# Kernel optimization log

Hardware: AMD Instinct MI355X
Metric: run time of the kernel (lower is better)

## Reference

```python
import jax, jax.numpy as jnp
import numpy as np

D_MODEL = 2048
N_HEADS = 16
N_KV_HEADS = 2
HEAD_DIM = D_MODEL // N_HEADS  # 128
N_REP = N_HEADS // N_KV_HEADS  # 8
SCALE = HEAD_DIM ** -0.5


def setup_inputs() -> dict:
    key = jax.random.key(0)
    ks = jax.random.split(key, 5)
    B, N = 2, 2048
    x = jax.random.normal(ks[0], (B, N, D_MODEL), dtype=jnp.float32)
    # weights stored as [in, out] (math identical to torch Linear x @ W.T)
    s = D_MODEL ** -0.5
    Wq = jax.random.normal(ks[1], (D_MODEL, D_MODEL), dtype=jnp.float32) * s
    Wk = jax.random.normal(ks[2], (D_MODEL, N_KV_HEADS * HEAD_DIM), dtype=jnp.float32) * s
    Wv = jax.random.normal(ks[3], (D_MODEL, N_KV_HEADS * HEAD_DIM), dtype=jnp.float32) * s
    Wo = jax.random.normal(ks[4], (D_MODEL, D_MODEL), dtype=jnp.float32) * s
    return {"x": x, "Wq": Wq, "Wk": Wk, "Wv": Wv, "Wo": Wo}


def reference(x, Wq, Wk, Wv, Wo):
    B, N, C = x.shape
    q = (x @ Wq).reshape(B, N, N_HEADS, HEAD_DIM).transpose(0, 2, 1, 3)      # [B,H,N,hd]
    k = (x @ Wk).reshape(B, N, N_KV_HEADS, HEAD_DIM).transpose(0, 2, 1, 3)   # [B,Hkv,N,hd]
    v = (x @ Wv).reshape(B, N, N_KV_HEADS, HEAD_DIM).transpose(0, 2, 1, 3)
    if N_REP > 1:
        k = jnp.repeat(k, N_REP, axis=1)  # [B,H,N,hd]
        v = jnp.repeat(v, N_REP, axis=1)
    attn = jnp.einsum('bhnd,bhmd->bhnm', q, k) * SCALE
    attn = jax.nn.softmax(attn, axis=-1)
    out = jnp.einsum('bhnm,bhmd->bhnd', attn, v)
    out = out.transpose(0, 2, 1, 3).reshape(B, N, C)
    return out @ Wo
```

## Files before the change

kernel.cpp:

```cpp
#include <hip/hip_runtime.h>

typedef unsigned short u16;
typedef __attribute__((ext_vector_type(4))) float floatx4;
typedef __attribute__((ext_vector_type(8))) __bf16 bf16x8;
typedef __attribute__((ext_vector_type(8))) u16 u16x8;

#define D_MODEL 2048
#define SEQ     2048
#define NH      16
#define NKV     2
#define HD      128
#define QKVN    2560
#define SCALE   0.08838834764831845f
#define QSCALE  (0.08838834764831845f * 1.4426950408889634f)
#define M_STATIC 20.0f

__device__ __forceinline__ u16 f2bf(float f) {
    unsigned int x = __float_as_uint(f);
    return (u16)((x + 0x7fffu + ((x >> 16) & 1u)) >> 16);
}
__device__ __forceinline__ u16 cvt_scale(float f, float s) { return f2bf(f * s); }
__device__ __forceinline__ u16 cvt_scale(u16 f, float)     { return f; }

__device__ __forceinline__ void gload16(const u16* g, u16* l) {
    __builtin_amdgcn_global_load_lds((const __attribute__((address_space(1))) void*)g,
                                     (__attribute__((address_space(3))) void*)l, 16, 0, 0);
}

__global__ void f2b_k(const float* __restrict__ src, u16* __restrict__ dst, long n)
{
    long i = ((long)blockIdx.x * blockDim.x + threadIdx.x) * 8;
    if (i >= n) return;
    float4 a = *(const float4*)(src + i);
    float4 b = *(const float4*)(src + i + 4);
    u16x8 o;
    o[0] = f2bf(a.x); o[1] = f2bf(a.y); o[2] = f2bf(a.z); o[3] = f2bf(a.w);
    o[4] = f2bf(b.x); o[5] = f2bf(b.y); o[6] = f2bf(b.z); o[7] = f2bf(b.w);
    *(u16x8*)(dst + i) = o;
}

template <typename T>
__global__ void tr_k(const T* __restrict__ src, u16* __restrict__ dst,
                     int ld_s, int ld_d, long sbs, long dbs, float scale)
{
    __shared__ T tile[32][33];
    src += (long)blockIdx.z * sbs;
    dst += (long)blockIdx.z * dbs;
    int c0 = blockIdx.x * 32, r0 = blockIdx.y * 32;
    int tx = threadIdx.x, ty = threadIdx.y;
#pragma unroll
    for (int i = 0; i < 32; i += 8)
        tile[ty + i][tx] = src[(long)(r0 + ty + i) * ld_s + c0 + tx];
    __syncthreads();
#pragma unroll
    for (int i = 0; i < 32; i += 8)
        dst[(long)(c0 + ty + i) * ld_d + r0 + tx] = cvt_scale(tile[tx][ty + i], scale);
}

template <bool F32OUT>
__global__ __launch_bounds__(256, 2) void gemm_bt_k(
    const u16* __restrict__ A, const u16* __restrict__ Bt, void* __restrict__ Cv,
    int K, int lda, int ldb, int ldc)
{
    __shared__ __align__(16) u16 As[128 * 64];
    __shared__ __align__(16) u16 Bs[128 * 64];
    const int tid  = threadIdx.x;
    const int wave = tid >> 6, lane = tid & 63;
    const int quad = lane >> 4, l16 = lane & 15;
    const long bm = (long)blockIdx.x * 128;
    const long bn = (long)blockIdx.y * 128;
    const int wr = (wave >> 1) * 64;
    const int wc = (wave & 1) * 64;

    floatx4 acc[4][4] = {};

    for (long k0 = 0; k0 < K; k0 += 64) {
#pragma unroll
        for (int t = 0; t < 4; ++t) {
            int c = tid + t * 256;
            int row = c >> 3, sl = c & 7;
            int kc = sl ^ (row & 7);
            gload16(A + (bm + row) * lda + k0 + kc * 8,
                    As + ((tid & ~63) + t * 256) * 8);
        }
#pragma unroll
        for (int t = 0; t < 4; ++t) {
            int c = tid + t * 256;
            int row = c >> 3, sl = c & 7;
            int kc = sl ^ (row & 7);
            gload16(Bt + (bn + row) * ldb + k0 + kc * 8,
                    Bs + ((tid & ~63) + t * 256) * 8);
        }
        __syncthreads();

#pragma unroll
        for (int ks = 0; ks < 2; ++ks) {
            bf16x8 af[4], bfr[4];
#pragma unroll
            for (int mt = 0; mt < 4; ++mt) {
                int r  = wr + mt * 16 + l16;
                int ch = (ks * 4 + quad) ^ (r & 7);
                af[mt] = *(const bf16x8*)(As + r * 64 + ch * 8);
            }
#pragma unroll
            for (int nt = 0; nt < 4; ++nt) {
                int r  = wc + nt * 16 + l16;
                int ch = (ks * 4 + quad) ^ (r & 7);
                bfr[nt] = *(const bf16x8*)(Bs + r * 64 + ch * 8);
            }
#pragma unroll
            for (int mt = 0; mt < 4; ++mt)
#pragma unroll
                for (int nt = 0; nt < 4; ++nt)
                    acc[mt][nt] = __builtin_amdgcn_mfma_f32_16x16x32_bf16(
                        af[mt], bfr[nt], acc[mt][nt], 0, 0, 0);
        }
        __syncthreads();
    }

#pragma unroll
    for (int mt = 0; mt < 4; ++mt)
#pragma unroll
        for (int nt = 0; nt < 4; ++nt)
#pragma unroll
            for (int r = 0; r < 4; ++r) {
                long row = bm + wr + mt * 16 + quad * 4 + r;
                long col = bn + wc + nt * 16 + l16;
                if (F32OUT) ((float*)Cv)[row * ldc + col] = acc[mt][nt][r];
                else        ((u16*)Cv)[row * ldc + col]   = f2bf(acc[mt][nt][r]);
            }
}

#define KTILE (64 * 128)
#define VTILE (128 * 64)
#define NT    (SEQ / 64)

__global__ __launch_bounds__(512, 2) void attn_k(
    const u16* __restrict__ QKV, const u16* __restrict__ Vt, u16* __restrict__ Out)
{
    __shared__ __align__(16) u16 smem[2 * KTILE + 2 * VTILE + 256 * 64];

    const int tid  = threadIdx.x;
    const int wave = tid >> 6, lane = tid & 63;
    const int quad = lane >> 4, l16 = lane & 15;
    const int qs = wave & 3;
    const int hf = wave >> 2;
    const int qt = blockIdx.x, h = blockIdx.y, b = blockIdx.z;
    const int kvh = h >> 3;

    const long qrow0 = (long)b * SEQ + (long)qt * 256;
    const u16* Qbase = QKV + qrow0 * QKVN + h * HD;
    const u16* Kbase = QKV + (long)b * SEQ * QKVN + D_MODEL + kvh * HD;
    const u16* Vbase = Vt + ((long)b * NKV + kvh) * (long)HD * SEQ;
    u16* const P = smem + 2 * KTILE + 2 * VTILE;

#pragma unroll
    for (int t = 0; t < 8; ++t) {
        int c = tid + t * 512;
        int row = c >> 4, sl = c & 15;
        int dc = sl ^ (row & 15);
        gload16(Qbase + (long)row * QKVN + dc * 8, smem + ((tid & ~63) + t * 512) * 8);
    }
    __syncthreads();

    bf16x8 qa[4][4];
#pragma unroll
    for (int mt = 0; mt < 4; ++mt)
#pragma unroll
        for (int ks = 0; ks < 4; ++ks) {
            int r  = qs * 64 + mt * 16 + l16;
            int ch = (ks * 4 + quad) ^ (r & 15);
            qa[mt][ks] = *(const bf16x8*)(smem + r * 128 + ch * 8);
        }
    __syncthreads();

    floatx4 o[4][4] = {};
    float l_run[4] = { 0.f, 0.f, 0.f, 0.f };

    {
        u16* Kn = smem;
        u16* Vn = smem + 2 * KTILE;
#pragma unroll
        for (int t = 0; t < 2; ++t) {
            int c = tid + t * 512;
            int row = c >> 4, sl = c & 15;
            int dc = sl ^ (row & 15);
            gload16(Kbase + (long)row * QKVN + dc * 8, Kn + ((tid & ~63) + t * 512) * 8);
        }
#pragma unroll
        for (int t = 0; t < 2; ++t) {
            int c = tid + t * 512;
            int row = c >> 3, sl = c & 7;
            int kc = sl ^ (row & 7);
            gload16(Vbase + (long)row * SEQ + kc * 8, Vn + ((tid & ~63) + t * 512) * 8);
        }
    }
    __syncthreads();

    for (int t = 0; t < NT; ++t) {
        const int cur = t & 1;
        const u16* Kc = smem + cur * KTILE;
        const u16* Vc = smem + 2 * KTILE + cur * VTILE;

        if (t + 1 < NT) {
            u16* Kn = smem + (cur ^ 1) * KTILE;
            u16* Vn = smem + 2 * KTILE + (cur ^ 1) * VTILE;
            const long k0n = (long)(t + 1) * 64;
#pragma unroll
            for (int tt = 0; tt < 2; ++tt) {
                int c = tid + tt * 512;
                int row = c >> 4, sl = c & 15;
                int dc = sl ^ (row & 15);
                gload16(Kbase + (k0n + row) * QKVN + dc * 8,
                        Kn + ((tid & ~63) + tt * 512) * 8);
            }
#pragma unroll
            for (int tt = 0; tt < 2; ++tt) {
                int c = tid + tt * 512;
                int row = c >> 3, sl = c & 7;
                int kc = sl ^ (row & 7);
                gload16(Vbase + (long)row * SEQ + k0n + kc * 8,
                        Vn + ((tid & ~63) + tt * 512) * 8);
            }
        }

        floatx4 s[4][2] = {};
        __builtin_amdgcn_s_setprio(1);
#pragma unroll
        for (int ks = 0; ks < 4; ++ks) {
            bf16x8 kb[2];
#pragma unroll
            for (int nt = 0; nt < 2; ++nt) {
                int r  = hf * 32 + nt * 16 + l16;
                int ch = (ks * 4 + quad) ^ (r & 15);
                kb[nt] = *(const bf16x8*)(Kc + r * 128 + ch * 8);
            }
#pragma unroll
            for (int mt = 0; mt < 4; ++mt)
#pragma unroll
                for (int nt = 0; nt < 2; ++nt)
                    s[mt][nt] = __builtin_amdgcn_mfma_f32_16x16x32_bf16(
                        kb[nt], qa[mt][ks], s[mt][nt], 0, 0, 0);
        }
        __builtin_amdgcn_s_setprio(0);

#pragma unroll
        for (int mt = 0; mt < 4; ++mt) {
#pragma unroll
            for (int nt = 0; nt < 2; ++nt)
#pragma unroll
                for (int r = 0; r < 4; ++r)
                    s[mt][nt][r] = __builtin_amdgcn_exp2f(s[mt][nt][r] - M_STATIC);
            float ta = (s[mt][0][0] + s[mt][0][1]) + (s[mt][0][2] + s[mt][0][3]);
            float tb = (s[mt][1][0] + s[mt][1][1]) + (s[mt][1][2] + s[mt][1][3]);
            float sum = ta + tb;
            sum += __shfl_xor(sum, 16);
            sum += __shfl_xor(sum, 32);
            l_run[mt] += sum;

            int row = qs * 64 + mt * 16 + l16;
            int m = row & 7;
            u16* base = P + row * 64 + (quad & 1) * 4;
#pragma unroll
            for (int nt = 0; nt < 2; ++nt) {
                unsigned int lo, hi;
                asm("v_cvt_pk_bf16_f32 %0, %1, %2"
                    : "=v"(lo) : "v"(s[mt][nt][0]), "v"(s[mt][nt][1]));
                asm("v_cvt_pk_bf16_f32 %0, %1, %2"
                    : "=v"(hi) : "v"(s[mt][nt][2]), "v"(s[mt][nt][3]));
                int chunk = (hf * 4 + nt * 2 + (quad >> 1)) ^ m;
                uint2 val; val.x = lo; val.y = hi;
                *(uint2*)(base + chunk * 8) = val;
            }
        }

        asm volatile("s_waitcnt lgkmcnt(0)" ::: "memory");
        __builtin_amdgcn_sched_barrier(0);
        __builtin_amdgcn_s_barrier();

        __builtin_amdgcn_s_setprio(1);
#pragma unroll
        for (int ks = 0; ks < 2; ++ks) {
            bf16x8 pa[4];
#pragma unroll
            for (int mt = 0; mt < 4; ++mt) {
                int row = qs * 64 + mt * 16 + l16;
                int chk = (ks * 4 + quad) ^ (row & 7);
                pa[mt] = *(const bf16x8*)(P + row * 64 + chk * 8);
            }
#pragma unroll
            for (int dt = 0; dt < 4; ++dt) {
                int r  = hf * 64 + dt * 16 + l16;
                int ch = (ks * 4 + quad) ^ (r & 7);
                bf16x8 vb = *(const bf16x8*)(Vc + r * 64 + ch * 8);
#pragma unroll
                for (int mt = 0; mt < 4; ++mt)
                    o[mt][dt] = __builtin_amdgcn_mfma_f32_16x16x32_bf16(
                        pa[mt], vb, o[mt][dt], 0, 0, 0);
            }
        }
        __builtin_amdgcn_s_setprio(0);
        __syncthreads();
    }

    float* lbuf = (float*)P;
    if (quad == 0) {
#pragma unroll
        for (int mt = 0; mt < 4; ++mt)
            lbuf[(qs * 2 + hf) * 64 + mt * 16 + l16] = l_run[mt];
    }
    __syncthreads();
#pragma unroll
    for (int mt = 0; mt < 4; ++mt)
#pragma unroll
        for (int r = 0; r < 4; ++r) {
            int qq = mt * 16 + quad * 4 + r;
            float lt = lbuf[(qs * 2) * 64 + qq] + lbuf[(qs * 2 + 1) * 64 + qq];
            float inv = 1.f / lt;
            long row = qrow0 + qs * 64 + qq;
#pragma unroll
            for (int dt = 0; dt < 4; ++dt)
                Out[row * D_MODEL + h * HD + hf * 64 + dt * 16 + l16] =
                    f2bf(o[mt][dt][r] * inv);
        }
}

extern "C" void kernel_launch(void* const* d_in, const int* in_sizes, int n_in,
                              void* d_out, int out_size, void* d_ws, size_t ws_size,
                              hipStream_t stream)
{
    const float* X  = (const float*)d_in[0];
    const float* Wq = (const float*)d_in[1];
    const float* Wk = (const float*)d_in[2];
    const float* Wv = (const float*)d_in[3];
    const float* Wo = (const float*)d_in[4];
    float* out = (float*)d_out;

    u16* Xb    = (u16*)d_ws;
    u16* attn  = Xb;
    u16* WtQKV = Xb + (long)4096 * D_MODEL;
    u16* WtO   = WtQKV + (long)QKVN * D_MODEL;
    u16* QKV   = WtO + (long)D_MODEL * D_MODEL;
    u16* Vt    = QKV + (long)4096 * QKVN;

    f2b_k<<<dim3(4096), 256, 0, stream>>>(X, Xb, (long)4096 * D_MODEL);

    dim3 tb(32, 8);
    tr_k<float><<<dim3(64, 64, 1), tb, 0, stream>>>(Wq, WtQKV, 2048, 2048, 0, 0, QSCALE);
    tr_k<float><<<dim3(8, 64, 1), tb, 0, stream>>>(Wk, WtQKV + 2048L * 2048, 256, 2048, 0, 0, 1.f);
    tr_k<float><<<dim3(8, 64, 1), tb, 0, stream>>>(Wv, WtQKV + 2304L * 2048, 256, 2048, 0, 0, 1.f);
    tr_k<float><<<dim3(64, 64, 1), tb, 0, stream>>>(Wo, WtO, 2048, 2048, 0, 0, 1.f);

    gemm_bt_k<false><<<dim3(32, 20), 256, 0, stream>>>(Xb, WtQKV, QKV, 2048, 2048, 2048, QKVN);

    tr_k<u16><<<dim3(8, 64, 2), tb, 0, stream>>>(QKV + 2304, Vt, QKVN, 2048,
                                                 (long)SEQ * QKVN, 256L * 2048, 1.f);

    attn_k<<<dim3(8, NH, 2), 512, 0, stream>>>(QKV, Vt, attn);

    gemm_bt_k<true><<<dim3(32, 16), 256, 0, stream>>>(attn, WtO, out, 2048, 2048, 2048, 2048);
}
```

Before: 272.5 us.

## Software-pipeline attention loop so PV of previous tile overlaps QK of current tile

Restructures the attention main loop so each iteration computes QK^T for tile t and then the P·V product for tile t-1, with a final P·V epilogue after the loop. The P buffer is double-buffered, and the V load for a tile is now issued in the same iteration as its QK, a step before its P·V use. This cuts the loop to one barrier per iteration and lets softmax exp work interleave with matrix ops. The cost is more LDS (about 128 KB per block instead of 96 KB), which likely allows only one 512-thread block per CU instead of the two that launch_bounds requests.

```diff
diff --git a/kernel.cpp b/kernel.cpp
--- a/kernel.cpp
+++ b/kernel.cpp
@@ -133,12 +133,13 @@
 
 #define KTILE (64 * 128)
 #define VTILE (128 * 64)
+#define PTILE (256 * 64)
 #define NT    (SEQ / 64)
 
 __global__ __launch_bounds__(512, 2) void attn_k(
     const u16* __restrict__ QKV, const u16* __restrict__ Vt, u16* __restrict__ Out)
 {
-    __shared__ __align__(16) u16 smem[2 * KTILE + 2 * VTILE + 256 * 64];
+    __shared__ __align__(16) u16 smem[2 * KTILE + 2 * VTILE + 2 * PTILE];
 
     const int tid  = threadIdx.x;
     const int wave = tid >> 6, lane = tid & 63;
@@ -152,7 +153,12 @@
     const u16* Qbase = QKV + qrow0 * QKVN + h * HD;
     const u16* Kbase = QKV + (long)b * SEQ * QKVN + D_MODEL + kvh * HD;
     const u16* Vbase = Vt + ((long)b * NKV + kvh) * (long)HD * SEQ;
-    u16* const P = smem + 2 * KTILE + 2 * VTILE;
+    u16* const K0 = smem;
+    u16* const K1 = smem + KTILE;
+    u16* const V0 = smem + 2 * KTILE;
+    u16* const V1 = smem + 2 * KTILE + VTILE;
+    u16* const P0 = smem + 2 * KTILE + 2 * VTILE;
+    u16* const P1 = P0 + PTILE;
 
 #pragma unroll
     for (int t = 0; t < 8; ++t) {
@@ -176,35 +182,26 @@
 
     floatx4 o[4][4] = {};
     float l_run[4] = { 0.f, 0.f, 0.f, 0.f };
-
-    {
-        u16* Kn = smem;
-        u16* Vn = smem + 2 * KTILE;
-#pragma unroll
-        for (int t = 0; t < 2; ++t) {
-            int c = tid + t * 512;
-            int row = c >> 4, sl = c & 15;
-            int dc = sl ^ (row & 15);
-            gload16(Kbase + (long)row * QKVN + dc * 8, Kn + ((tid & ~63) + t * 512) * 8);
-        }
-#pragma unroll
-        for (int t = 0; t < 2; ++t) {
-            int c = tid + t * 512;
-            int row = c >> 3, sl = c & 7;
-            int kc = sl ^ (row & 7);
-            gload16(Vbase + (long)row * SEQ + kc * 8, Vn + ((tid & ~63) + t * 512) * 8);
-        }
-    }
-    __syncthreads();
+    floatx4 s[4][2];
+
+#pragma unroll
+    for (int t = 0; t < 2; ++t) {
+        int c = tid + t * 512;
+        int row = c >> 4, sl = c & 15;
+        int dc = sl ^ (row & 15);
+        gload16(Kbase + (long)row * QKVN + dc * 8, K0 + ((tid & ~63) + t * 512) * 8);
+    }
 
     for (int t = 0; t < NT; ++t) {
-        const int cur = t & 1;
-        const u16* Kc = smem + cur * KTILE;
-        const u16* Vc = smem + 2 * KTILE + cur * VTILE;
+        __syncthreads();
+        u16* const Kc = (t & 1) ? K1 : K0;
+        u16* const Ka = (t & 1) ? K0 : K1;
+        u16* const Vc = (t & 1) ? V1 : V0;
+        u16* const Vp = (t & 1) ? V0 : V1;
+        u16* const Pc = (t & 1) ? P1 : P0;
+        u16* const Pp = (t & 1) ? P0 : P1;
 
         if (t + 1 < NT) {
-            u16* Kn = smem + (cur ^ 1) * KTILE;
-            u16* Vn = smem + 2 * KTILE + (cur ^ 1) * VTILE;
             const long k0n = (long)(t + 1) * 64;
 #pragma unroll
             for (int tt = 0; tt < 2; ++tt) {
@@ -212,20 +209,27 @@
                 int row = c >> 4, sl = c & 15;
                 int dc = sl ^ (row & 15);
                 gload16(Kbase + (k0n + row) * QKVN + dc * 8,
-                        Kn + ((tid & ~63) + tt * 512) * 8);
-            }
+                        Ka + ((tid & ~63) + tt * 512) * 8);
+            }
+        }
+        {
+            const long k0v = (long)t * 64;
 #pragma unroll
             for (int tt = 0; tt < 2; ++tt) {
                 int c = tid + tt * 512;
                 int row = c >> 3, sl = c & 7;
                 int kc = sl ^ (row & 7);
-                gload16(Vbase + (long)row * SEQ + k0n + kc * 8,
-                        Vn + ((tid & ~63) + tt * 512) * 8);
-            }
-        }
-
-        floatx4 s[4][2] = {};
+                gload16(Vbase + (long)row * SEQ + k0v + kc * 8,
+                        Vc + ((tid & ~63) + tt * 512) * 8);
+            }
+        }
+
         __builtin_amdgcn_s_setprio(1);
+#pragma unroll
+        for (int mt = 0; mt < 4; ++mt)
+#pragma unroll
+            for (int nt = 0; nt < 2; ++nt)
+                s[mt][nt] = floatx4{0.f, 0.f, 0.f, 0.f};
 #pragma unroll
         for (int ks = 0; ks < 4; ++ks) {
             bf16x8 kb[2];
@@ -241,6 +245,29 @@
                 for (int nt = 0; nt < 2; ++nt)
                     s[mt][nt] = __builtin_amdgcn_mfma_f32_16x16x32_bf16(
                         kb[nt], qa[mt][ks], s[mt][nt], 0, 0, 0);
+        }
+
+        if (t > 0) {
+#pragma unroll
+            for (int ks = 0; ks < 2; ++ks) {
+                bf16x8 pa[4];
+#pragma unroll
+                for (int mt = 0; mt < 4; ++mt) {
+                    int row = qs * 64 + mt * 16 + l16;
+                    int chk = (ks * 4 + quad) ^ (row & 7);
+                    pa[mt] = *(const bf16x8*)(Pp + row * 64 + chk * 8);
+                }
+#pragma unroll
+                for (int dt = 0; dt < 4; ++dt) {
+                    int r  = hf * 64 + dt * 16 + l16;
+                    int ch = (ks * 4 + quad) ^ (r & 7);
+                    bf16x8 vb = *(const bf16x8*)(Vp + r * 64 + ch * 8);
+#pragma unroll
+                    for (int mt = 0; mt < 4; ++mt)
+                        o[mt][dt] = __builtin_amdgcn_mfma_f32_16x16x32_bf16(
+                            pa[mt], vb, o[mt][dt], 0, 0, 0);
+                }
+            }
         }
         __builtin_amdgcn_s_setprio(0);
 
@@ -260,7 +287,7 @@
 
             int row = qs * 64 + mt * 16 + l16;
             int m = row & 7;
-            u16* base = P + row * 64 + (quad & 1) * 4;
+            u16* base = Pc + row * 64 + (quad & 1) * 4;
 #pragma unroll
             for (int nt = 0; nt < 2; ++nt) {
                 unsigned int lo, hi;
@@ -273,12 +300,12 @@
                 *(uint2*)(base + chunk * 8) = val;
             }
         }
-
-        asm volatile("s_waitcnt lgkmcnt(0)" ::: "memory");
-        __builtin_amdgcn_sched_barrier(0);
-        __builtin_amdgcn_s_barrier();
-
-        __builtin_amdgcn_s_setprio(1);
+    }
+
+    __syncthreads();
+    {
+        u16* const Pp = ((NT - 1) & 1) ? P1 : P0;
+        u16* const Vp = ((NT - 1) & 1) ? V1 : V0;
 #pragma unroll
         for (int ks = 0; ks < 2; ++ks) {
             bf16x8 pa[4];
@@ -286,24 +313,22 @@
             for (int mt = 0; mt < 4; ++mt) {
                 int row = qs * 64 + mt * 16 + l16;
                 int chk = (ks * 4 + quad) ^ (row & 7);
-                pa[mt] = *(const bf16x8*)(P + row * 64 + chk * 8);
+                pa[mt] = *(const bf16x8*)(Pp + row * 64 + chk * 8);
             }
 #pragma unroll
             for (int dt = 0; dt < 4; ++dt) {
                 int r  = hf * 64 + dt * 16 + l16;
                 int ch = (ks * 4 + quad) ^ (r & 7);
-                bf16x8 vb = *(const bf16x8*)(Vc + r * 64 + ch * 8);
+                bf16x8 vb = *(const bf16x8*)(Vp + r * 64 + ch * 8);
 #pragma unroll
                 for (int mt = 0; mt < 4; ++mt)
                     o[mt][dt] = __builtin_amdgcn_mfma_f32_16x16x32_bf16(
                         pa[mt], vb, o[mt][dt], 0, 0, 0);
             }
         }
-        __builtin_amdgcn_s_setprio(0);
-        __syncthreads();
-    }
-
-    float* lbuf = (float*)P;
+    }
+
+    float* lbuf = (float*)K0;
     if (quad == 0) {
 #pragma unroll
         for (int mt = 0; mt < 4; ++mt)
```

Result: slower. 279.2 us (+2.5%).
